# Kernel tuning notes

Hardware: AMD Instinct MI355X
Metric: run time of the kernel (lower is better)

Reference implementation:

```python
import jax, jax.numpy as jnp
import numpy as np

N = 100000  # nodes per type (user, tweet)
E = 500000  # edges per relation
D = 128     # input feature dim
H = 128     # hidden dim


def _seg_mean(h_src, src, dst, n_dst):
    # DGL copy_u + mean: mean of source features over incoming edges; zero for in-degree 0.
    msg = h_src[src]                                                    # [E, F] gather
    s = jax.ops.segment_sum(msg, dst, num_segments=n_dst)               # [n_dst, F] scatter-add
    cnt = jax.ops.segment_sum(jnp.ones((src.shape[0], 1), h_src.dtype), dst, num_segments=n_dst)
    return s / jnp.maximum(cnt, 1.0)


def setup_inputs() -> dict:
    key = jax.random.key(0)
    ks = jax.random.split(key, 24)
    f = lambda i, shp, s=1.0: jax.random.normal(ks[i], shp, dtype=jnp.float32) * s
    return {
        'x_user': f(0, (N, D)), 'x_tweet': f(1, (N, D)),
        # layer 1, relation 'posts' (user -> tweet) and 'posted_by' (tweet -> user)
        'w1ps': f(2, (H, D), 0.05), 'b1ps': f(3, (H,), 0.05),
        'w1pn': f(4, (H, D), 0.05), 'b1pn': f(5, (H,), 0.05),
        'w1bs': f(6, (H, D), 0.05), 'b1bs': f(7, (H,), 0.05),
        'w1bn': f(8, (H, D), 0.05), 'b1bn': f(9, (H,), 0.05),
        # layer 2 (out_feats = 1, no activation)
        'w2ps': f(10, (1, H), 0.05), 'b2ps': f(11, (1,), 0.05),
        'w2pn': f(12, (1, H), 0.05), 'b2pn': f(13, (1,), 0.05),
        'w2bs': f(14, (1, H), 0.05), 'b2bs': f(15, (1,), 0.05),
        'w2bn': f(16, (1, H), 0.05), 'b2bn': f(17, (1,), 0.05),
        'src_posts': jax.random.randint(ks[18], (E,), 0, N),
        'dst_posts': jax.random.randint(ks[19], (E,), 0, N),
        'src_pb': jax.random.randint(ks[20], (E,), 0, N),
        'dst_pb': jax.random.randint(ks[21], (E,), 0, N),
    }


def reference(x_user, x_tweet,
              w1ps, b1ps, w1pn, b1pn, w1bs, b1bs, w1bn, b1bn,
              w2ps, b2ps, w2pn, b2pn, w2bs, b2bs, w2bn, b2bn,
              src_posts, dst_posts, src_pb, dst_pb):
    # ---- conv1: DivFeatConv per relation, relu, cross-relation sum (one rel per dst type) ----
    neigh_t = _seg_mean(x_user, src_posts, dst_posts, N)               # user -posts-> tweet
    h_tweet = jax.nn.relu(x_tweet @ w1ps.T + b1ps + neigh_t @ w1pn.T + b1pn)
    neigh_u = _seg_mean(x_tweet, src_pb, dst_pb, N)                    # tweet -posted_by-> user
    h_user = jax.nn.relu(x_user @ w1bs.T + b1bs + neigh_u @ w1bn.T + b1bn)
    # ---- conv2: out_feats=1, identity activation ----
    neigh_t2 = _seg_mean(h_user, src_posts, dst_posts, N)
    out_tweet = h_tweet @ w2ps.T + b2ps + neigh_t2 @ w2pn.T + b2pn     # [N, 1]
    neigh_u2 = _seg_mean(h_tweet, src_pb, dst_pb, N)
    out_user = h_user @ w2bs.T + b2bs + neigh_u2 @ w2bn.T + b2bn       # [N, 1]
    return (out_user, out_tweet)
```

## Files before the change

kernel.cpp:

```cpp
#include <hip/hip_runtime.h>

#define N_NODES 100000
#define N_EDGES 500000
#define DIM 128

typedef __attribute__((ext_vector_type(8))) short short8;
typedef __attribute__((ext_vector_type(4))) float f32x4;

__device__ __forceinline__ ushort f2bf(float f) {
    unsigned u = __float_as_uint(f);
    u += 0x7FFF + ((u >> 16) & 1);
    return (ushort)(u >> 16);
}
__device__ __forceinline__ float bf2f(ushort s) {
    return __uint_as_float(((unsigned)s) << 16);
}


__global__ __launch_bounds__(256) void build_lists2_kernel(
    const int* __restrict__ s0, const int* __restrict__ d0,
    const int* __restrict__ s1, const int* __restrict__ d1,
    int* __restrict__ head2, int2* __restrict__ entry2) {
    const int rel = blockIdx.y;
    const int* src = rel ? s1 : s0;
    const int* dst = rel ? d1 : d0;
    int* head = head2 + rel * N_NODES;
    int2* entry = entry2 + (size_t)rel * N_EDGES;
    int e = blockIdx.x * 256 + threadIdx.x;
    if (e < N_EDGES) {
        int d = dst[e];
        int old = atomicExch(&head[d], e);
        entry[e] = make_int2(src[e], old);
    }
}


__global__ __launch_bounds__(256) void cvtw_kernel(
    const float* __restrict__ w0, const float* __restrict__ w1,
    const float* __restrict__ w2, const float* __restrict__ w3,
    ushort* __restrict__ o0, ushort* __restrict__ o1,
    ushort* __restrict__ o2, ushort* __restrict__ o3) {
    int a = blockIdx.y;
    const float* in = (a == 0) ? w0 : (a == 1) ? w1 : (a == 2) ? w2 : w3;
    ushort* out = (a == 0) ? o0 : (a == 1) ? o1 : (a == 2) ? o2 : o3;
    int i = (blockIdx.x * 256 + threadIdx.x) * 4;
    float4 v = *reinterpret_cast<const float4*>(&in[i]);
    ushort4 u = make_ushort4(f2bf(v.x), f2bf(v.y), f2bf(v.z), f2bf(v.w));
    *reinterpret_cast<ushort4*>(&out[i]) = u;
}

__global__ __launch_bounds__(256) void cvtx_kernel(const float* __restrict__ x0,
                                                   const float* __restrict__ x1,
                                                   ushort* __restrict__ o0,
                                                   ushort* __restrict__ o1) {
    const float* in = blockIdx.y ? x1 : x0;
    ushort* out = blockIdx.y ? o1 : o0;
    int i = (blockIdx.x * 256 + threadIdx.x) * 4;
    float4 v = *reinterpret_cast<const float4*>(&in[i]);
    ushort4 u = make_ushort4(f2bf(v.x), f2bf(v.y), f2bf(v.z), f2bf(v.w));
    *reinterpret_cast<ushort4*>(&out[i]) = u;
}


__global__ __launch_bounds__(256) void seg_mean_bf16_list_kernel(
    const ushort* __restrict__ x, const int* __restrict__ head,
    const int2* __restrict__ entry, ushort* __restrict__ outbf) {
    int idx = blockIdx.x * 256 + threadIdx.x;
    int node = idx >> 4;
    if (node >= N_NODES) return;
    int f = (idx & 15) << 3;
    float acc[8];
#pragma unroll
    for (int j = 0; j < 8; ++j) acc[j] = 0.f;
    int cnt = 0;
    int e = head[node];
    while (e >= 0) {
        int2 nd = entry[e];
        ++cnt;
        short8 v = *reinterpret_cast<const short8*>(&x[(size_t)nd.x * DIM + f]);
#pragma unroll
        for (int j = 0; j < 8; ++j) acc[j] += bf2f((ushort)v[j]);
        e = nd.y;
    }
    float r = 1.0f / fmaxf((float)cnt, 1.0f);
    union { ushort s[8]; uint4 v; } u;
#pragma unroll
    for (int j = 0; j < 8; ++j) u.s[j] = f2bf(acc[j] * r);
    *reinterpret_cast<uint4*>(&outbf[(size_t)node * DIM + f]) = u.v;
}

__global__ __launch_bounds__(256) void seg_mean_f32_list_kernel(
    const float* __restrict__ x, const int* __restrict__ head,
    const int2* __restrict__ entry, ushort* __restrict__ outbf) {
    int idx = blockIdx.x * 256 + threadIdx.x;
    int node = idx >> 5;
    if (node >= N_NODES) return;
    int f = (idx & 31) << 2;
    float4 acc = make_float4(0.f, 0.f, 0.f, 0.f);
    int cnt = 0;
    int e = head[node];
    while (e >= 0) {
        int2 nd = entry[e];
        ++cnt;
        float4 v = *reinterpret_cast<const float4*>(&x[(size_t)nd.x * DIM + f]);
        acc.x += v.x; acc.y += v.y; acc.z += v.z; acc.w += v.w;
        e = nd.y;
    }
    float r = 1.0f / fmaxf((float)cnt, 1.0f);
    ushort4 u = make_ushort4(f2bf(acc.x * r), f2bf(acc.y * r),
                             f2bf(acc.z * r), f2bf(acc.w * r));
    *reinterpret_cast<ushort4*>(&outbf[(size_t)node * DIM + f]) = u;
}

__global__ __launch_bounds__(256) void scalar_seg2_list_kernel(
    const float* __restrict__ sv0, const float* __restrict__ sv1,
    const int* __restrict__ head2, const int2* __restrict__ entry2,
    float* __restrict__ sm0, float* __restrict__ sm1) {
    const int rel = blockIdx.y;
    const float* sval = rel ? sv1 : sv0;
    const int* head = head2 + rel * N_NODES;
    const int2* entry = entry2 + (size_t)rel * N_EDGES;
    float* smean = rel ? sm1 : sm0;
    int node = blockIdx.x * 256 + threadIdx.x;
    if (node >= N_NODES) return;
    float a = 0.f;
    int cnt = 0;
    int e = head[node];
    while (e >= 0) {
        int2 nd = entry[e];
        ++cnt;
        a += sval[nd.x];
        e = nd.y;
    }
    smean[node] = a / fmaxf((float)cnt, 1.0f);
}

__global__ __launch_bounds__(256) void gemm_mfma_kernel(
    const float* __restrict__ Xs,
    const ushort* __restrict__ Nm,
    const ushort* __restrict__ Wsbf,
    const ushort* __restrict__ Wnbf,
    const float* __restrict__ bs, const float* __restrict__ bn,
    const float* __restrict__ w2a, const float* __restrict__ w2b,
    float* __restrict__ dself, float* __restrict__ dcross) {
    __shared__ ushort sA[128 * 64];
    __shared__ ushort sB[128 * 64];
    __shared__ float pS[2][2][128];

    const int tid = threadIdx.x;
    const int lane = tid & 63;
    const int wid = tid >> 6;
    const int wr = wid >> 1, wc = wid & 1;
    const int lr = lane & 15, lg = lane >> 4;
    const int row0 = blockIdx.x * 128;

    f32x4 acc[4][4];
#pragma unroll
    for (int i = 0; i < 4; ++i)
#pragma unroll
        for (int j = 0; j < 4; ++j) acc[i][j] = (f32x4){0.f, 0.f, 0.f, 0.f};

    const int r = tid >> 1;
    const int hh = tid & 1;
    const int grow = row0 + r;
    const int swzr = (r & 7) << 4;

    for (int kb = 0; kb < 256; kb += 64) {
        const int kg = kb & 127;
        const bool self = (kb < 128);
        __syncthreads();
        if (self) {
            const float4* g = reinterpret_cast<const float4*>(Xs);
#pragma unroll
            for (int q = 0; q < 4; ++q) {
                float4 v0 = make_float4(0.f, 0.f, 0.f, 0.f), v1 = v0;
                if (grow < N_NODES) {
                    size_t bi = ((size_t)grow * DIM + kg + hh * 32 + q * 8) >> 2;
                    v0 = g[bi];
                    v1 = g[bi + 1];
                }
                union { ushort s[8]; uint4 v; } u;
                u.s[0] = f2bf(v0.x); u.s[1] = f2bf(v0.y);
                u.s[2] = f2bf(v0.z); u.s[3] = f2bf(v0.w);
                u.s[4] = f2bf(v1.x); u.s[5] = f2bf(v1.y);
                u.s[6] = f2bf(v1.z); u.s[7] = f2bf(v1.w);
                int byte = (hh * 64 + q * 16) ^ swzr;
                *reinterpret_cast<uint4*>(&sA[r * 64 + (byte >> 1)]) = u.v;
            }
        } else {
            const uint4* g = reinterpret_cast<const uint4*>(Nm);
#pragma unroll
            for (int q = 0; q < 4; ++q) {
                uint4 v = make_uint4(0, 0, 0, 0);
                if (grow < N_NODES)
                    v = g[((size_t)grow * DIM + kg + hh * 32 + q * 8) >> 3];
                int byte = (hh * 64 + q * 16) ^ swzr;
                *reinterpret_cast<uint4*>(&sA[r * 64 + (byte >> 1)]) = v;
            }
        }
        {
            const uint4* g = reinterpret_cast<const uint4*>(self ? Wsbf : Wnbf);
#pragma unroll
            for (int q = 0; q < 4; ++q) {
                uint4 v = g[(r * DIM + kg + hh * 32 + q * 8) >> 3];
                int byte = (hh * 64 + q * 16) ^ swzr;
                *reinterpret_cast<uint4*>(&sB[r * 64 + (byte >> 1)]) = v;
            }
        }
        __syncthreads();
#pragma unroll
        for (int ks = 0; ks < 2; ++ks) {
            short8 a[4], b[4];
#pragma unroll
            for (int fm = 0; fm < 4; ++fm) {
                int rr = wr * 64 + fm * 16 + lr;
                int byte = (ks * 64 + lg * 16) ^ ((rr & 7) << 4);
                a[fm] = *reinterpret_cast<const short8*>(&sA[rr * 64 + (byte >> 1)]);
            }
#pragma unroll
            for (int fn = 0; fn < 4; ++fn) {
                int cc = wc * 64 + fn * 16 + lr;
                int byte = (ks * 64 + lg * 16) ^ ((cc & 7) << 4);
                b[fn] = *reinterpret_cast<const short8*>(&sB[cc * 64 + (byte >> 1)]);
            }
#pragma unroll
            for (int fm = 0; fm < 4; ++fm)
#pragma unroll
                for (int fn = 0; fn < 4; ++fn)
                    acc[fm][fn] = __builtin_amdgcn_mfma_f32_16x16x32_bf16(
                        a[fm], b[fn], acc[fm][fn], 0, 0, 0);
        }
    }

    float bias[4], wa[4], wb[4];
#pragma unroll
    for (int fn = 0; fn < 4; ++fn) {
        int c = wc * 64 + fn * 16 + lr;
        bias[fn] = bs[c] + bn[c];
        wa[fn] = w2a[c];
        wb[fn] = w2b[c];
    }
#pragma unroll
    for (int fm = 0; fm < 4; ++fm) {
#pragma unroll
        for (int reg = 0; reg < 4; ++reg) {
            float pa = 0.f, pb = 0.f;
#pragma unroll
            for (int fn = 0; fn < 4; ++fn) {
                float h = fmaxf(acc[fm][fn][reg] + bias[fn], 0.f);
                pa = fmaf(h, wa[fn], pa);
                pb = fmaf(h, wb[fn], pb);
            }
#pragma unroll
            for (int m = 1; m < 16; m <<= 1) {
                pa += __shfl_xor(pa, m);
                pb += __shfl_xor(pb, m);
            }
            if (lr == 0) {
                int rloc = wr * 64 + fm * 16 + lg * 4 + reg;
                pS[wc][0][rloc] = pa;
                pS[wc][1][rloc] = pb;
            }
        }
    }
    __syncthreads();
    if (tid < 128) {
        int go = row0 + tid;
        if (go < N_NODES) {
            dself[go] = pS[0][0][tid] + pS[1][0][tid];
            dcross[go] = pS[0][1][tid] + pS[1][1][tid];
        }
    }
}

__global__ __launch_bounds__(256) void finalize_kernel(
    const float* __restrict__ dself_u, const float* __restrict__ smean_u,
    const float* __restrict__ b2bs, const float* __restrict__ b2bn,
    const float* __restrict__ dself_t, const float* __restrict__ smean_t,
    const float* __restrict__ b2ps, const float* __restrict__ b2pn,
    float* __restrict__ out) {
    int i = blockIdx.x * 256 + threadIdx.x;
    if (i >= N_NODES) return;
    out[i] = dself_u[i] + smean_u[i] + b2bs[0] + b2bn[0];
    out[N_NODES + i] = dself_t[i] + smean_t[i] + b2ps[0] + b2pn[0];
}

extern "C" void kernel_launch(void* const* d_in, const int* in_sizes, int n_in,
                              void* d_out, int out_size, void* d_ws, size_t ws_size,
                              hipStream_t stream) {
    const float* x_user  = (const float*)d_in[0];
    const float* x_tweet = (const float*)d_in[1];
    const float* w1ps = (const float*)d_in[2];  const float* b1ps = (const float*)d_in[3];
    const float* w1pn = (const float*)d_in[4];  const float* b1pn = (const float*)d_in[5];
    const float* w1bs = (const float*)d_in[6];  const float* b1bs = (const float*)d_in[7];
    const float* w1bn = (const float*)d_in[8];  const float* b1bn = (const float*)d_in[9];
    const float* w2ps = (const float*)d_in[10]; const float* b2ps = (const float*)d_in[11];
    const float* w2pn = (const float*)d_in[12]; const float* b2pn = (const float*)d_in[13];
    const float* w2bs = (const float*)d_in[14]; const float* b2bs = (const float*)d_in[15];
    const float* w2bn = (const float*)d_in[16]; const float* b2bn = (const float*)d_in[17];
    const int* src_posts = (const int*)d_in[18];
    const int* dst_posts = (const int*)d_in[19];
    const int* src_pb    = (const int*)d_in[20];
    const int* dst_pb    = (const int*)d_in[21];
    float* out = (float*)d_out;

    char* wsb = (char*)d_ws;
    ushort* nbf     = (ushort*)wsb;   wsb += (size_t)N_NODES * DIM * 2;
    int* head2      = (int*)wsb;      wsb += (size_t)2 * N_NODES * 4;
    int2* entry2    = (int2*)wsb;     wsb += (size_t)2 * N_EDGES * 8;
    ushort* wbf_ps  = (ushort*)wsb;   wsb += (size_t)DIM * DIM * 2;
    ushort* wbf_pn  = (ushort*)wsb;   wsb += (size_t)DIM * DIM * 2;
    ushort* wbf_bs  = (ushort*)wsb;   wsb += (size_t)DIM * DIM * 2;
    ushort* wbf_bn  = (ushort*)wsb;   wsb += (size_t)DIM * DIM * 2;
    float* dself_t  = (float*)wsb;    wsb += (size_t)N_NODES * 4;
    float* scross_t = (float*)wsb;    wsb += (size_t)N_NODES * 4;
    float* dself_u  = (float*)wsb;    wsb += (size_t)N_NODES * 4;
    float* scross_u = (float*)wsb;    wsb += (size_t)N_NODES * 4;
    float* smean_t  = (float*)wsb;    wsb += (size_t)N_NODES * 4;
    float* smean_u  = (float*)wsb;    wsb += (size_t)N_NODES * 4;
    ushort* xbf_u   = (ushort*)wsb;   wsb += (size_t)N_NODES * DIM * 2;
    ushort* xbf_t   = (ushort*)wsb;   wsb += (size_t)N_NODES * DIM * 2;
    const bool use_bf = ((size_t)(wsb - (char*)d_ws) <= ws_size);

    const int* head_posts = head2;
    const int* head_pb    = head2 + N_NODES;
    const int2* ent_posts = entry2;
    const int2* ent_pb    = entry2 + N_EDGES;

    const int gE = (N_EDGES + 255) / 256;
    const int gN = (N_NODES + 255) / 256;
    const int gG = (N_NODES + 127) / 128;

    cvtw_kernel<<<dim3(16, 4), 256, 0, stream>>>(w1ps, w1pn, w1bs, w1bn,
                                                 wbf_ps, wbf_pn, wbf_bs, wbf_bn);
    if (use_bf)
        cvtx_kernel<<<dim3(12500, 2), 256, 0, stream>>>(x_user, x_tweet, xbf_u, xbf_t);

    hipMemsetAsync(head2, 0xFF, 2 * N_NODES * sizeof(int), stream);
    build_lists2_kernel<<<dim3(gE, 2), 256, 0, stream>>>(src_posts, dst_posts,
                                                         src_pb, dst_pb, head2, entry2);

    if (use_bf)
        seg_mean_bf16_list_kernel<<<(N_NODES * 16 + 255) / 256, 256, 0, stream>>>(
            xbf_u, head_posts, ent_posts, nbf);
    else
        seg_mean_f32_list_kernel<<<(N_NODES * 32 + 255) / 256, 256, 0, stream>>>(
            x_user, head_posts, ent_posts, nbf);
    gemm_mfma_kernel<<<gG, 256, 0, stream>>>(x_tweet, nbf, wbf_ps, wbf_pn,
                                             b1ps, b1pn, w2ps, w2bn, dself_t, scross_t);

    if (use_bf)
        seg_mean_bf16_list_kernel<<<(N_NODES * 16 + 255) / 256, 256, 0, stream>>>(
            xbf_t, head_pb, ent_pb, nbf);
    else
        seg_mean_f32_list_kernel<<<(N_NODES * 32 + 255) / 256, 256, 0, stream>>>(
            x_tweet, head_pb, ent_pb, nbf);
    gemm_mfma_kernel<<<gG, 256, 0, stream>>>(x_user, nbf, wbf_bs, wbf_bn,
                                             b1bs, b1bn, w2bs, w2pn, dself_u, scross_u);

    scalar_seg2_list_kernel<<<dim3(gN, 2), 256, 0, stream>>>(scross_u, scross_t,
                                                             head2, entry2,
                                                             smean_t, smean_u);

    finalize_kernel<<<gN, 256, 0, stream>>>(dself_u, smean_u, b2bs, b2bn,
                                            dself_t, smean_t, b2ps, b2pn, out);
}
```

Before: 223.1 us.

## Pad list heads, use bf16 self features in GEMM, fuse scalar mean into finalize

Spreads the per-node list heads to a stride of four ints so that concurrent atomic exchanges from neighbouring destinations land on fewer shared cache lines. Adds a GEMM variant that reads the already converted bf16 self features instead of fp32, which halves the A-operand load traffic. Merges the scalar segment mean with the finalize kernel to drop one launch and the intermediate buffers. In exchange, head reads during traversal become strided and less coalesced, and the memset grows fourfold.

Result: faster. 211.4 us (-5.2%).

```diff
diff --git a/kernel.cpp b/kernel.cpp
--- a/kernel.cpp
+++ b/kernel.cpp
@@ -3,6 +3,7 @@
 #define N_NODES 100000
 #define N_EDGES 500000
 #define DIM 128
+#define HSTR 4
 
 typedef __attribute__((ext_vector_type(8))) short short8;
 typedef __attribute__((ext_vector_type(4))) float f32x4;
@@ -24,12 +25,12 @@
     const int rel = blockIdx.y;
     const int* src = rel ? s1 : s0;
     const int* dst = rel ? d1 : d0;
-    int* head = head2 + rel * N_NODES;
+    int* head = head2 + (size_t)rel * N_NODES * HSTR;
     int2* entry = entry2 + (size_t)rel * N_EDGES;
     int e = blockIdx.x * 256 + threadIdx.x;
     if (e < N_EDGES) {
         int d = dst[e];
-        int old = atomicExch(&head[d], e);
+        int old = atomicExch(&head[(size_t)d * HSTR], e);
         entry[e] = make_int2(src[e], old);
     }
 }
@@ -73,7 +74,7 @@
 #pragma unroll
     for (int j = 0; j < 8; ++j) acc[j] = 0.f;
     int cnt = 0;
-    int e = head[node];
+    int e = head[(size_t)node * HSTR];
     while (e >= 0) {
         int2 nd = entry[e];
         ++cnt;
@@ -98,7 +99,7 @@
     int f = (idx & 31) << 2;
     float4 acc = make_float4(0.f, 0.f, 0.f, 0.f);
     int cnt = 0;
-    int e = head[node];
+    int e = head[(size_t)node * HSTR];
     while (e >= 0) {
         int2 nd = entry[e];
         ++cnt;
@@ -109,37 +110,132 @@
     float r = 1.0f / fmaxf((float)cnt, 1.0f);
     ushort4 u = make_ushort4(f2bf(acc.x * r), f2bf(acc.y * r),
                              f2bf(acc.z * r), f2bf(acc.w * r));
-    *reinterpret_cast<ushort4*>(&outbf[(size_t)node * DIM + f]) = u;
-}
-
-__global__ __launch_bounds__(256) void scalar_seg2_list_kernel(
-    const float* __restrict__ sv0, const float* __restrict__ sv1,
-    const int* __restrict__ head2, const int2* __restrict__ entry2,
-    float* __restrict__ sm0, float* __restrict__ sm1) {
-    const int rel = blockIdx.y;
-    const float* sval = rel ? sv1 : sv0;
-    const int* head = head2 + rel * N_NODES;
-    const int2* entry = entry2 + (size_t)rel * N_EDGES;
-    float* smean = rel ? sm1 : sm0;
-    int node = blockIdx.x * 256 + threadIdx.x;
-    if (node >= N_NODES) return;
-    float a = 0.f;
-    int cnt = 0;
-    int e = head[node];
-    while (e >= 0) {
-        int2 nd = entry[e];
-        ++cnt;
-        a += sval[nd.x];
-        e = nd.y;
-    }
-    smean[node] = a / fmaxf((float)cnt, 1.0f);
-}
-
-__global__ __launch_bounds__(256) void gemm_mfma_kernel(
-    const float* __restrict__ Xs,
+    *reinterpret_cast<ushort4*>(&outbf[node * DIM + f]) = u;
+}
+
+__global__ __launch_bounds__(256) void gemm_mfma_bf_kernel(
+    const ushort* __restrict__ Xsbf,
     const ushort* __restrict__ Nm,
     const ushort* __restrict__ Wsbf,
     const ushort* __restrict__ Wnbf,
+    const float* __restrict__ bs, const float* __restrict__ bn,
+    const float* __restrict__ w2a, const float* __restrict__ w2b,
+    float* __restrict__ dself, float* __restrict__ dcross) {
+    __shared__ ushort sA[128 * 64];
+    __shared__ ushort sB[128 * 64];
+    __shared__ float pS[2][2][128];
+
+    const int tid = threadIdx.x;
+    const int lane = tid & 63;
+    const int wid = tid >> 6;
+    const int wr = wid >> 1, wc = wid & 1;
+    const int lr = lane & 15, lg = lane >> 4;
+    const int row0 = blockIdx.x * 128;
+
+    f32x4 acc[4][4];
+#pragma unroll
+    for (int i = 0; i < 4; ++i)
+#pragma unroll
+        for (int j = 0; j < 4; ++j) acc[i][j] = (f32x4){0.f, 0.f, 0.f, 0.f};
+
+    const int r = tid >> 1;
+    const int hh = tid & 1;
+    const int grow = row0 + r;
+    const int swzr = (r & 7) << 4;
+
+    for (int kb = 0; kb < 256; kb += 64) {
+        const int kg = kb & 127;
+        const bool self = (kb < 128);
+        __syncthreads();
+        {
+            const uint4* g = reinterpret_cast<const uint4*>(self ? Xsbf : Nm);
+#pragma unroll
+            for (int q = 0; q < 4; ++q) {
+                uint4 v = make_uint4(0, 0, 0, 0);
+                if (grow < N_NODES)
+                    v = g[((size_t)grow * DIM + kg + hh * 32 + q * 8) >> 3];
+                int byte = (hh * 64 + q * 16) ^ swzr;
+                *reinterpret_cast<uint4*>(&sA[r * 64 + (byte >> 1)]) = v;
+            }
+        }
+        {
+            const uint4* g = reinterpret_cast<const uint4*>(self ? Wsbf : Wnbf);
+#pragma unroll
+            for (int q = 0; q < 4; ++q) {
+                uint4 v = g[(r * DIM + kg + hh * 32 + q * 8) >> 3];
+                int byte = (hh * 64 + q * 16) ^ swzr;
+                *reinterpret_cast<uint4*>(&sB[r * 64 + (byte >> 1)]) = v;
+            }
+        }
+        __syncthreads();
+#pragma unroll
+        for (int ks = 0; ks < 2; ++ks) {
+            short8 a[4], b[4];
+#pragma unroll
+            for (int fm = 0; fm < 4; ++fm) {
+                int rr = wr * 64 + fm * 16 + lr;
+                int byte = (ks * 64 + lg * 16) ^ ((rr & 7) << 4);
+                a[fm] = *reinterpret_cast<const short8*>(&sA[rr * 64 + (byte >> 1)]);
+            }
+#pragma unroll
+            for (int fn = 0; fn < 4; ++fn) {
+                int cc = wc * 64 + fn * 16 + lr;
+                int byte = (ks * 64 + lg * 16) ^ ((cc & 7) << 4);
+                b[fn] = *reinterpret_cast<const short8*>(&sB[cc * 64 + (byte >> 1)]);
+            }
+#pragma unroll
+            for (int fm = 0; fm < 4; ++fm)
+#pragma unroll
+                for (int fn = 0; fn < 4; ++fn)
+                    acc[fm][fn] = __builtin_amdgcn_mfma_f32_16x16x32_bf16(
+                        a[fm], b[fn], acc[fm][fn], 0, 0, 0);
+        }
+    }
+
+    float bias[4], wa[4], wb[4];
+#pragma unroll
+    for (int fn = 0; fn < 4; ++fn) {
+        int c = wc * 64 + fn * 16 + lr;
+        bias[fn] = bs[c] + bn[c];
+        wa[fn] = w2a[c];
+        wb[fn] = w2b[c];
+    }
+#pragma unroll
+    for (int fm = 0; fm < 4; ++fm) {
+#pragma unroll
+        for (int reg = 0; reg < 4; ++reg) {
+            float pa = 0.f, pb = 0.f;
+#pragma unroll
+            for (int fn = 0; fn < 4; ++fn) {
+                float h = fmaxf(acc[fm][fn][reg] + bias[fn], 0.f);
+                pa = fmaf(h, wa[fn], pa);
+                pb = fmaf(h, wb[fn], pb);
+            }
+#pragma unroll
+            for (int m = 1; m < 16; m <<= 1) {
+                pa += __shfl_xor(pa, m);
+                pb += __shfl_xor(pb, m);
+            }
+            if (lr == 0) {
+                int rloc = wr * 64 + fm * 16 + lg * 4 + reg;
+                pS[wc][0][rloc] = pa;
+                pS[wc][1][rloc] = pb;
+            }
+        }
+    }
+    __syncthreads();
+    if (tid < 128) {
+        int go = row0 + tid;
+        if (go < N_NODES) {
+            dself[go] = pS[0][0][tid] + pS[1][0][tid];
+            dcross[go] = pS[0][1][tid] + pS[1][1][tid];
+        }
+    }
+}
+
+__global__ __launch_bounds__(256) void gemm_mfma_kernel(
+    const float* __restrict__ Xs, const ushort* __restrict__ Nm,
+    const ushort* __restrict__ Wsbf, const ushort* __restrict__ Wnbf,
     const float* __restrict__ bs, const float* __restrict__ bn,
     const float* __restrict__ w2a, const float* __restrict__ w2b,
     float* __restrict__ dself, float* __restrict__ dcross) {
@@ -273,16 +369,37 @@
     }
 }
 
-__global__ __launch_bounds__(256) void finalize_kernel(
-    const float* __restrict__ dself_u, const float* __restrict__ smean_u,
+__global__ __launch_bounds__(256) void scalar_finalize_kernel(
+    const float* __restrict__ dself_u, const float* __restrict__ dself_t,
+    const float* __restrict__ scross_u, const float* __restrict__ scross_t,
+    const int* __restrict__ head2, const int2* __restrict__ entry2,
     const float* __restrict__ b2bs, const float* __restrict__ b2bn,
-    const float* __restrict__ dself_t, const float* __restrict__ smean_t,
     const float* __restrict__ b2ps, const float* __restrict__ b2pn,
     float* __restrict__ out) {
     int i = blockIdx.x * 256 + threadIdx.x;
     if (i >= N_NODES) return;
-    out[i] = dself_u[i] + smean_u[i] + b2bs[0] + b2bn[0];
-    out[N_NODES + i] = dself_t[i] + smean_t[i] + b2ps[0] + b2pn[0];
+    {
+        float a = 0.f; int cnt = 0;
+        int e = head2[(size_t)i * HSTR];
+        while (e >= 0) {
+            int2 nd = entry2[e];
+            ++cnt;
+            a += scross_u[nd.x];
+            e = nd.y;
+        }
+        out[N_NODES + i] = dself_t[i] + a / fmaxf((float)cnt, 1.0f) + b2ps[0] + b2pn[0];
+    }
+    {
+        float a = 0.f; int cnt = 0;
+        int e = head2[((size_t)N_NODES + i) * HSTR];
+        while (e >= 0) {
+            int2 nd = entry2[(size_t)N_EDGES + e];
+            ++cnt;
+            a += scross_t[nd.x];
+            e = nd.y;
+        }
+        out[i] = dself_u[i] + a / fmaxf((float)cnt, 1.0f) + b2bs[0] + b2bn[0];
+    }
 }
 
 extern "C" void kernel_launch(void* const* d_in, const int* in_sizes, int n_in,
@@ -306,7 +423,7 @@
 
     char* wsb = (char*)d_ws;
     ushort* nbf     = (ushort*)wsb;   wsb += (size_t)N_NODES * DIM * 2;
-    int* head2      = (int*)wsb;      wsb += (size_t)2 * N_NODES * 4;
+    int* head2      = (int*)wsb;      wsb += (size_t)2 * N_NODES * HSTR * 4;
     int2* entry2    = (int2*)wsb;     wsb += (size_t)2 * N_EDGES * 8;
     ushort* wbf_ps  = (ushort*)wsb;   wsb += (size_t)DIM * DIM * 2;
     ushort* wbf_pn  = (ushort*)wsb;   wsb += (size_t)DIM * DIM * 2;
@@ -316,14 +433,12 @@
     float* scross_t = (float*)wsb;    wsb += (size_t)N_NODES * 4;
     float* dself_u  = (float*)wsb;    wsb += (size_t)N_NODES * 4;
     float* scross_u = (float*)wsb;    wsb += (size_t)N_NODES * 4;
-    float* smean_t  = (float*)wsb;    wsb += (size_t)N_NODES * 4;
-    float* smean_u  = (float*)wsb;    wsb += (size_t)N_NODES * 4;
     ushort* xbf_u   = (ushort*)wsb;   wsb += (size_t)N_NODES * DIM * 2;
     ushort* xbf_t   = (ushort*)wsb;   wsb += (size_t)N_NODES * DIM * 2;
     const bool use_bf = ((size_t)(wsb - (char*)d_ws) <= ws_size);
 
     const int* head_posts = head2;
-    const int* head_pb    = head2 + N_NODES;
+    const int* head_pb    = head2 + (size_t)N_NODES * HSTR;
     const int2* ent_posts = entry2;
     const int2* ent_pb    = entry2 + N_EDGES;
 
@@ -336,32 +451,39 @@
     if (use_bf)
         cvtx_kernel<<<dim3(12500, 2), 256, 0, stream>>>(x_user, x_tweet, xbf_u, xbf_t);
 
-    hipMemsetAsync(head2, 0xFF, 2 * N_NODES * sizeof(int), stream);
+    hipMemsetAsync(head2, 0xFF, (size_t)2 * N_NODES * HSTR * sizeof(int), stream);
     build_lists2_kernel<<<dim3(gE, 2), 256, 0, stream>>>(src_posts, dst_posts,
                                                          src_pb, dst_pb, head2, entry2);
 
-    if (use_bf)
+    if (use_bf) {
         seg_mean_bf16_list_kernel<<<(N_NODES * 16 + 255) / 256, 256, 0, stream>>>(
             xbf_u, head_posts, ent_posts, nbf);
-    else
+        gemm_mfma_bf_kernel<<<gG, 256, 0, stream>>>(xbf_t, nbf, wbf_ps, wbf_pn,
+                                                    b1ps, b1pn, w2ps, w2bn,
+                                                    dself_t, scross_t);
+    } else {
         seg_mean_f32_list_kernel<<<(N_NODES * 32 + 255) / 256, 256, 0, stream>>>(
             x_user, head_posts, ent_posts, nbf);
-    gemm_mfma_kernel<<<gG, 256, 0, stream>>>(x_tweet, nbf, wbf_ps, wbf_pn,
-                                             b1ps, b1pn, w2ps, w2bn, dself_t, scross_t);
-
-    if (use_bf)
+        gemm_mfma_kernel<<<gG, 256, 0, stream>>>(x_tweet, nbf, wbf_ps, wbf_pn,
+                                                 b1ps, b1pn, w2ps, w2bn,
+                                                 dself_t, scross_t);
+    }
+
+    if (use_bf) {
         seg_mean_bf16_list_kernel<<<(N_NODES * 16 + 255) / 256, 256, 0, stream>>>(
             xbf_t, head_pb, ent_pb, nbf);
-    else
+        gemm_mfma_bf_kernel<<<gG, 256, 0, stream>>>(xbf_u, nbf, wbf_bs, wbf_bn,
+                                                    b1bs, b1bn, w2bs, w2pn,
+                                                    dself_u, scross_u);
+    } else {
         seg_mean_f32_list_kernel<<<(N_NODES * 32 + 255) / 256, 256, 0, stream>>>(
             x_tweet, head_pb, ent_pb, nbf);
-    gemm_mfma_kernel<<<gG, 256, 0, stream>>>(x_user, nbf, wbf_bs, wbf_bn,
-                                             b1bs, b1bn, w2bs, w2pn, dself_u, scross_u);
-
-    scalar_seg2_list_kernel<<<dim3(gN, 2), 256, 0, stream>>>(scross_u, scross_t,
-                                                             head2, entry2,
-                                                             smean_t, smean_u);
-
-    finalize_kernel<<<gN, 256, 0, stream>>>(dself_u, smean_u, b2bs, b2bn,
-                                            dself_t, smean_t, b2ps, b2pn, out);
-}
+        gemm_mfma_kernel<<<gG, 256, 0, stream>>>(x_user, nbf, wbf_bs, wbf_bn,
+                                                 b1bs, b1bn, w2bs, w2pn,
+                                                 dself_u, scross_u);
+    }
+
+    scalar_finalize_kernel<<<gN, 256, 0, stream>>>(dself_u, dself_t, scross_u, scross_t,
+                                                   head2, entry2, b2bs, b2bn, b2ps, b2pn,
+                                                   out);
+}
```
